# Kernel optimization log

Measured on AMD Instinct MI355X. Metric: run time of the kernel, lower is better.

The kernel has to match this reference:

```python
import jax, jax.numpy as jnp
import numpy as np

L_KERNELS = 15
STRIDE = 1
DIMS = [60, 72, 86, 86, 71, 59]  # indim=4*15, then *1.2,*1.2, mid, /1.2,/1.2 per __init__


def setup_inputs() -> dict:
    key = jax.random.key(0)
    ks = jax.random.split(key, 13)
    B, C, L, K = 16, 4, 1000, 64
    inp = {"x": jax.random.normal(ks[0], (B, C, L), jnp.float32)}
    for i in range(5):
        di, do = DIMS[i], DIMS[i + 1]
        inp[f"w{i}"] = jax.random.normal(ks[1 + 2 * i], (K, di, do), jnp.float32) * (1.0 / np.sqrt(di))
        inp[f"b{i}"] = jax.random.normal(ks[2 + 2 * i], (K, do), jnp.float32) * 0.01
    inp["head_w"] = jax.random.normal(ks[11], (DIMS[5], 1), jnp.float32) * (1.0 / np.sqrt(DIMS[5]))
    inp["head_b"] = jax.random.normal(ks[12], (1,), jnp.float32) * 0.01
    return inp


def reference(x, w0, b0, w1, b1, w2, b2, w3, b3, w4, b4, head_w, head_b):
    B, C, L = x.shape
    l, s = L_KERNELS, STRIDE
    n_out = (L - l) // s + 1
    # unfold: (B, C, n_out, l) via gather of sliding windows
    idx = jnp.arange(n_out)[:, None] * s + jnp.arange(l)[None, :]
    xw = x[:, :, idx]
    # transpose(-2,-3) then flatten(start_dim=3): (B, n_out, C*l)
    xw = jnp.transpose(xw, (0, 2, 1, 3)).reshape(B, n_out, C * l)
    # per-kernel FC stack: broadcast-mul+sum in torch == grouped matmul here
    h = jax.nn.gelu(jnp.einsum('bld,kde->bkle', xw, w0) + b0[None, :, None, :], approximate=False)
    for w, b in ((w1, b1), (w2, b2), (w3, b3), (w4, b4)):
        h = jax.nn.gelu(jnp.einsum('bkld,kde->bkle', h, w) + b[None, :, None, :], approximate=False)
    out = (h @ head_w + head_b).squeeze(-1)  # (B, K, n_out)
    return out
```

## Files before the change

### kernel.cpp

```cpp
#include <hip/hip_runtime.h>

typedef _Float16 f16;
typedef __attribute__((ext_vector_type(8))) _Float16 f16x8;
typedef __attribute__((ext_vector_type(2))) __fp16 hf16x2;
typedef __attribute__((ext_vector_type(4))) float f32x4;

constexpr int C_ = 4, L_ = 1000, K_ = 64, NOUT = 986, NPOS = 16 * 986;
constexpr int TPB  = 256;
constexpr int MTB  = 128;
constexpr int NBLK = (NPOS + MTB - 1) / MTB;
constexpr int AST  = 104;
constexpr int ACT_EL  = MTB * AST;
constexpr size_t SMEM_BYTES = (size_t)ACT_EL * 2 + 480 * 4 + 64 * 4;

constexpr size_t WOFF[5]  = {0, 638976, 1277952, 1916928, 2555904};
constexpr int    WROWS[5] = {80, 96, 96, 80, 64};
constexpr int    DIv[5]   = {60, 72, 86, 86, 71};
constexpr int    DOv[5]   = {72, 86, 86, 71, 59};
constexpr size_t WTOT    = WOFF[4] + (size_t)K_ * 96 * AST;
constexpr size_t ACT_WS  = WTOT;
constexpr size_t WS_NEED = (WTOT + (size_t)NBLK * ACT_EL) * 2;

__device__ __forceinline__ float gelu_f(float x) {
    float x2 = x * x;
    float ei = x * __builtin_fmaf(-0.1029433270f, x2, -2.3022082020f);
    float e  = __builtin_amdgcn_exp2f(ei);
    return x * __builtin_amdgcn_rcpf(e + 1.0f);
}

template<int MT>
__device__ __forceinline__ void pre_a(const f16* __restrict__ wsrc, f16x8 (&ap)[6],
                                      int li, int q) {
#pragma unroll
    for (int mt = 0; mt < MT; mt++)
        ap[mt] = *(const f16x8*)(wsrc + (mt * 16 + li) * AST + q * 8);
}

template<int KSTEPS, int MT>
__device__ __forceinline__ void layer_mm_p(const f16* __restrict__ actw,
                                           const f16* __restrict__ wsrc,
                                           const f16x8 (&ap)[6],
                                           f32x4 (&acc)[MT][2],
                                           const float* __restrict__ bl, int li, int q) {
#pragma unroll
    for (int mt = 0; mt < MT; mt++) {
        f32x4 bb = *(const f32x4*)(bl + mt * 16 + q * 4);
#pragma unroll
        for (int nt = 0; nt < 2; nt++) acc[mt][nt] = bb;
    }
#pragma unroll
    for (int ks = 0; ks < KSTEPS; ks++) {
        const int koff = ks * 32 + q * 8;
        f16x8 a[MT], b[2];
#pragma unroll
        for (int mt = 0; mt < MT; mt++)
            a[mt] = (ks == 0) ? ap[mt]
                              : *(const f16x8*)(wsrc + (mt * 16 + li) * AST + koff);
#pragma unroll
        for (int nt = 0; nt < 2; nt++)
            b[nt] = *(const f16x8*)(actw + (nt * 16 + li) * AST + koff);
#pragma unroll
        for (int mt = 0; mt < MT; mt++)
#pragma unroll
            for (int nt = 0; nt < 2; nt++)
                acc[mt][nt] = __builtin_amdgcn_mfma_f32_16x16x32_f16(a[mt], b[nt], acc[mt][nt], 0, 0, 0);
    }
}

template<int MT>
__device__ __forceinline__ void epilogue(f32x4 (&acc)[MT][2], f16* __restrict__ actw,
                                         int li, int q) {
#pragma unroll
    for (int mt = 0; mt < MT; mt++) {
        const int eb = mt * 16 + q * 4;
#pragma unroll
        for (int nt = 0; nt < 2; nt++) {
            union { hf16x2 h[2]; unsigned long long u; } pk;
            pk.h[0] = __builtin_amdgcn_cvt_pkrtz(gelu_f(acc[mt][nt][0]),
                                                 gelu_f(acc[mt][nt][1]));
            pk.h[1] = __builtin_amdgcn_cvt_pkrtz(gelu_f(acc[mt][nt][2]),
                                                 gelu_f(acc[mt][nt][3]));
            f16* dst = actw + (nt * 16 + li) * AST + eb;
            *(unsigned long long*)dst = pk.u;
        }
    }
}

template<int L>
__device__ __forceinline__ void prep_one(const float* __restrict__ wsrc0, f16* __restrict__ ws,
                                         f16* __restrict__ wl, int k, int tid) {
    constexpr int DI = DIv[L], DO = DOv[L], RW = WROWS[L];
    const float* wsrc = wsrc0 + (size_t)k * DI * DO;
    constexpr int TOT = DI * DO;
    constexpr int NIT = (TOT + 255) / 256;
    float v[NIT];
#pragma unroll
    for (int it = 0; it < NIT; it++) {
        int i = tid + it * 256;
        v[it] = (i < TOT) ? wsrc[i] : 0.f;
    }
#pragma unroll
    for (int it = 0; it < NIT; it++) {
        int i = tid + it * 256;
        if (i < TOT) {
            int d = i / DO, e = i - d * DO;
            wl[d * 87 + e] = (f16)v[it];
        }
    }
    __syncthreads();
    f16* dst = ws + WOFF[L] + (size_t)k * 96 * AST;
    constexpr int CH = RW * 13;
    constexpr int NIT2 = (CH + 255) / 256;
#pragma unroll
    for (int it = 0; it < NIT2; it++) {
        int c = tid + it * 256;
        if (c < CH) {
            int e = c / 13, db = (c - e * 13) * 8;
            f16x8 vv;
#pragma unroll
            for (int j = 0; j < 8; j++) {
                int d = db + j;
                vv[j] = (e < DO && d < DI) ? wl[d * 87 + e] : (f16)0.f;
            }
            *(f16x8*)(dst + (size_t)c * 8) = vv;
        }
    }
}

__device__ __forceinline__ void prep_act(const float* __restrict__ x, f16* __restrict__ dst0,
                                         int m, int tid) {
    f16* dst = dst0 + (size_t)m * ACT_EL;
    const int base = m * MTB;
    for (int i = tid; i < ACT_EL; i += 256) {
        int r = i / AST, c = i - r * AST;
        int p = base + r; if (p > NPOS - 1) p = NPOS - 1;
        int b = p / NOUT, pos = p - b * NOUT;
        float v = 0.f;
        if (c < 60) { int ch = c / 15, j = c - ch * 15; v = x[(size_t)(b * C_ + ch) * L_ + pos + j]; }
        dst[i] = (f16)v;
    }
}

__global__ __launch_bounds__(256) void prep_weights(
    const float* __restrict__ w0, const float* __restrict__ w1, const float* __restrict__ w2,
    const float* __restrict__ w3, const float* __restrict__ w4,
    const float* __restrict__ x, f16* __restrict__ ws) {
    __shared__ f16 wl[86 * 87];
    const int tid = threadIdx.x;
    if (blockIdx.y == 5) { prep_act(x, ws + ACT_WS, blockIdx.x, tid); return; }
    const int k = blockIdx.x;
    if (k >= K_) return;
    switch (blockIdx.y) {
        case 0: prep_one<0>(w0, ws, wl, k, tid); break;
        case 1: prep_one<1>(w1, ws, wl, k, tid); break;
        case 2: prep_one<2>(w2, ws, wl, k, tid); break;
        case 3: prep_one<3>(w3, ws, wl, k, tid); break;
        default: prep_one<4>(w4, ws, wl, k, tid); break;
    }
}

template<bool PRE>
__global__ __launch_bounds__(TPB, 4) void mlp_main(
    const float* __restrict__ x,
    const float* __restrict__ b0, const float* __restrict__ b1, const float* __restrict__ b2,
    const float* __restrict__ b3, const float* __restrict__ b4,
    const float* __restrict__ hw, const float* __restrict__ hb,
    const f16* __restrict__ ws, float* __restrict__ out) {
    extern __shared__ char smemraw[];
    f16*   act   = (f16*)smemraw;
    float* biasl = (float*)(act + ACT_EL);
    float* headl = biasl + 480;

    const int tid = threadIdx.x, k = blockIdx.x, mblk = blockIdx.y;
    const int wv = tid >> 6, lane = tid & 63, li = lane & 15, q = lane >> 4;
    const int base = mblk * MTB;
    f16* actw = act + (wv * 32) * AST;
    const f16* wk = ws + (size_t)k * 96 * AST;

    f16x8 ap[6];
    pre_a<5>(wk + WOFF[0], ap, li, q);

    for (int i = tid; i < 480; i += TPB) {
        int l = i / 96, e = i - l * 96;
        const float* bg = (l == 0) ? b0 : (l == 1) ? b1 : (l == 2) ? b2 : (l == 3) ? b3 : b4;
        int DO = (l == 0) ? 72 : (l == 1) ? 86 : (l == 2) ? 86 : (l == 3) ? 71 : 59;
        biasl[i] = (e < DO) ? bg[k * DO + e] : 0.f;
    }
    if (tid < 64) headl[tid] = (tid < 59) ? hw[tid] : 0.f;

    if constexpr (PRE) {
        const f16* src = ws + ACT_WS + (size_t)mblk * ACT_EL;
        for (int c = wv; c < 26; c += 4) {
            __builtin_amdgcn_global_load_lds(
                (const __attribute__((address_space(1))) void*)(src + c * 512 + lane * 8),
                (__attribute__((address_space(3))) void*)(act + c * 512), 16, 0, 0);
        }
    } else {
        const int b0i = base / NOUT;
        const int thr = (b0i + 1) * NOUT;
        for (int i = tid; i < 64 * MTB; i += TPB) {
            int d = i >> 7, r = i & (MTB - 1);
            int p = base + r; if (p > NPOS - 1) p = NPOS - 1;
            int b = (p >= thr) ? b0i + 1 : b0i;
            int pos = p - b * NOUT;
            float v = 0.f;
            if (d < 60) { int c = d / 15, j = d - c * 15; v = x[(size_t)(b * C_ + c) * L_ + pos + j]; }
            act[r * AST + d] = (f16)v;
        }
        for (int i = tid; i < MTB * 2; i += TPB) {
            int r = i >> 1, cc = (i & 1) << 3;
            *(f16x8*)(act + r * AST + 80 + cc) = f16x8{0,0,0,0,0,0,0,0};
        }
    }
    const float hb0 = hb[0];
    __syncthreads();

    f32x4 acc[6][2];
    f32x4 (&acc5)[5][2] = reinterpret_cast<f32x4 (&)[5][2]>(acc);

    layer_mm_p<2, 5>(actw, wk + WOFF[0], ap, acc5, biasl + 0 * 96, li, q);
    pre_a<6>(wk + WOFF[1], ap, li, q);
    epilogue<5>(acc5, actw, li, q);
    layer_mm_p<3, 6>(actw, wk + WOFF[1], ap, acc, biasl + 1 * 96, li, q);
    pre_a<6>(wk + WOFF[2], ap, li, q);
    epilogue<6>(acc, actw, li, q);
    layer_mm_p<3, 6>(actw, wk + WOFF[2], ap, acc, biasl + 2 * 96, li, q);
    pre_a<5>(wk + WOFF[3], ap, li, q);
    epilogue<6>(acc, actw, li, q);
    layer_mm_p<3, 5>(actw, wk + WOFF[3], ap, acc5, biasl + 3 * 96, li, q);
    pre_a<4>(wk + WOFF[4], ap, li, q);
    epilogue<5>(acc5, actw, li, q);

    f32x4 acc4[4][2];
    layer_mm_p<3, 4>(actw, wk + WOFF[4], ap, acc4, biasl + 4 * 96, li, q);
    float sum[2] = {0.f, 0.f};
#pragma unroll
    for (int mt = 0; mt < 4; mt++) {
        const int eb = mt * 16 + q * 4;
        f32x4 hh = *(const f32x4*)(headl + eb);
#pragma unroll
        for (int nt = 0; nt < 2; nt++) {
#pragma unroll
            for (int r = 0; r < 4; r++)
                sum[nt] += gelu_f(acc4[mt][nt][r]) * hh[r];
        }
    }
#pragma unroll
    for (int nt = 0; nt < 2; nt++) {
        float s = sum[nt];
        s += __shfl_xor(s, 16);
        s += __shfl_xor(s, 32);
        s += hb0;
        if (lane < 16) {
            int p = base + wv * 32 + nt * 16 + lane;
            if (p < NPOS) {
                int b = p / NOUT, pos = p - b * NOUT;
                out[((size_t)(b * K_ + k)) * NOUT + pos] = s;
            }
        }
    }
}

extern "C" void kernel_launch(void* const* d_in, const int* in_sizes, int n_in,
                              void* d_out, int out_size, void* d_ws, size_t ws_size,
                              hipStream_t stream) {
    const float* x  = (const float*)d_in[0];
    const float* w0 = (const float*)d_in[1];  const float* b0 = (const float*)d_in[2];
    const float* w1 = (const float*)d_in[3];  const float* b1 = (const float*)d_in[4];
    const float* w2 = (const float*)d_in[5];  const float* b2 = (const float*)d_in[6];
    const float* w3 = (const float*)d_in[7];  const float* b3 = (const float*)d_in[8];
    const float* w4 = (const float*)d_in[9];  const float* b4 = (const float*)d_in[10];
    const float* hw = (const float*)d_in[11]; const float* hb = (const float*)d_in[12];
    float* out = (float*)d_out;
    f16* ws = (f16*)d_ws;

    const bool pre = (ws_size >= WS_NEED);

    if (pre) {
        (void)hipFuncSetAttribute((const void*)mlp_main<true>,
                                  hipFuncAttributeMaxDynamicSharedMemorySize, (int)SMEM_BYTES);
        prep_weights<<<dim3(NBLK, 6), 256, 0, stream>>>(w0, w1, w2, w3, w4, x, ws);
        mlp_main<true><<<dim3(K_, NBLK), TPB, SMEM_BYTES, stream>>>(
            x, b0, b1, b2, b3, b4, hw, hb, ws, out);
    } else {
        (void)hipFuncSetAttribute((const void*)mlp_main<false>,
                                  hipFuncAttributeMaxDynamicSharedMemorySize, (int)SMEM_BYTES);
        prep_weights<<<dim3(K_, 5), 256, 0, stream>>>(w0, w1, w2, w3, w4, x, ws);
        mlp_main<false><<<dim3(K_, NBLK), TPB, SMEM_BYTES, stream>>>(
            x, b0, b1, b2, b3, b4, hw, hb, ws, out);
    }
}
```

Before: 253.7 us.

## Fuse weight/activation prep and MLP into one persistent cooperative kernel

Replaces the two-launch sequence (prep kernel then main MLP kernel) with a single cooperative persistent kernel. Its blocks first convert weights and activations into the workspace, then do a grid-wide sync, then loop over row tiles with a fixed output channel k per block. The idea is to save a kernel launch and let each block keep its first-layer weight fragments in registers across tiles. It also vectorises activation prep into 8-wide f16 stores. The risks are the cost of the grid sync, less parallelism from the persistent grid being capped at 4 blocks per CU, and a possible occupancy-query failure at launch.

```diff
diff --git a/kernel.cpp b/kernel.cpp
--- a/kernel.cpp
+++ b/kernel.cpp
@@ -1,4 +1,7 @@
 #include <hip/hip_runtime.h>
+#include <hip/hip_cooperative_groups.h>
+
+namespace cg = cooperative_groups;
 
 typedef _Float16 f16;
 typedef __attribute__((ext_vector_type(8))) _Float16 f16x8;
@@ -20,6 +23,9 @@
 constexpr size_t WTOT    = WOFF[4] + (size_t)K_ * 96 * AST;
 constexpr size_t ACT_WS  = WTOT;
 constexpr size_t WS_NEED = (WTOT + (size_t)NBLK * ACT_EL) * 2;
+
+constexpr int NWUNIT = 5 * K_;
+constexpr int NPUNIT = NWUNIT + NBLK;
 
 __device__ __forceinline__ float gelu_f(float x) {
     float x2 = x * x;
@@ -129,15 +135,23 @@
 
 __device__ __forceinline__ void prep_act(const float* __restrict__ x, f16* __restrict__ dst0,
                                          int m, int tid) {
+    if (m >= NBLK) return;
     f16* dst = dst0 + (size_t)m * ACT_EL;
     const int base = m * MTB;
-    for (int i = tid; i < ACT_EL; i += 256) {
-        int r = i / AST, c = i - r * AST;
+    constexpr int CHK = MTB * 13;
+    for (int i = tid; i < CHK; i += 256) {
+        int r = i / 13, cc = (i - r * 13) * 8;
         int p = base + r; if (p > NPOS - 1) p = NPOS - 1;
         int b = p / NOUT, pos = p - b * NOUT;
-        float v = 0.f;
-        if (c < 60) { int ch = c / 15, j = c - ch * 15; v = x[(size_t)(b * C_ + ch) * L_ + pos + j]; }
-        dst[i] = (f16)v;
+        f16x8 vv;
+#pragma unroll
+        for (int j = 0; j < 8; j++) {
+            int c = cc + j;
+            float v = 0.f;
+            if (c < 60) { int ch = c / 15, jj = c - ch * 15; v = x[(size_t)(b * C_ + ch) * L_ + pos + jj]; }
+            vv[j] = (f16)v;
+        }
+        *(f16x8*)(dst + (size_t)r * AST + cc) = vv;
     }
 }
 
@@ -261,6 +275,118 @@
     }
 }
 
+__global__ __launch_bounds__(TPB, 4) void mlp_coop(
+    const float* __restrict__ x,
+    const float* __restrict__ w0, const float* __restrict__ w1, const float* __restrict__ w2,
+    const float* __restrict__ w3, const float* __restrict__ w4,
+    const float* __restrict__ b0, const float* __restrict__ b1, const float* __restrict__ b2,
+    const float* __restrict__ b3, const float* __restrict__ b4,
+    const float* __restrict__ hw, const float* __restrict__ hb,
+    f16* __restrict__ ws, float* __restrict__ out) {
+    extern __shared__ char smemraw[];
+    f16*   act   = (f16*)smemraw;
+    float* biasl = (float*)(act + ACT_EL);
+    float* headl = biasl + 480;
+
+    const int tid = threadIdx.x, bid = blockIdx.x, gsz = gridDim.x;
+
+    for (int u = bid; u < NPUNIT; u += gsz) {
+        if (u < NWUNIT) {
+            const int L = u >> 6, k2 = u & 63;
+            f16* wl = act;
+            switch (L) {
+                case 0: prep_one<0>(w0, ws, wl, k2, tid); break;
+                case 1: prep_one<1>(w1, ws, wl, k2, tid); break;
+                case 2: prep_one<2>(w2, ws, wl, k2, tid); break;
+                case 3: prep_one<3>(w3, ws, wl, k2, tid); break;
+                default: prep_one<4>(w4, ws, wl, k2, tid); break;
+            }
+        } else {
+            prep_act(x, ws + ACT_WS, u - NWUNIT, tid);
+        }
+        __syncthreads();
+    }
+
+    const int k = bid & 63;
+    for (int i = tid; i < 480; i += TPB) {
+        int l = i / 96, e = i - l * 96;
+        const float* bg = (l == 0) ? b0 : (l == 1) ? b1 : (l == 2) ? b2 : (l == 3) ? b3 : b4;
+        int DO = (l == 0) ? 72 : (l == 1) ? 86 : (l == 2) ? 86 : (l == 3) ? 71 : 59;
+        biasl[i] = (e < DO) ? bg[k * DO + e] : 0.f;
+    }
+    if (tid < 64) headl[tid] = (tid < 59) ? hw[tid] : 0.f;
+    const float hb0 = hb[0];
+
+    cg::this_grid().sync();
+
+    const int m0 = bid >> 6, mstep = gsz >> 6;
+    const int wv = tid >> 6, lane = tid & 63, li = lane & 15, q = lane >> 4;
+    f16* actw = act + (wv * 32) * AST;
+    const f16* wk = ws + (size_t)k * 96 * AST;
+
+    f16x8 ap[6];
+    pre_a<5>(wk + WOFF[0], ap, li, q);
+
+    for (int m = m0; m < NBLK; m += mstep) {
+        __syncthreads();
+        const f16* src = ws + ACT_WS + (size_t)m * ACT_EL;
+        for (int c = wv; c < 26; c += 4) {
+            __builtin_amdgcn_global_load_lds(
+                (const __attribute__((address_space(1))) void*)(src + c * 512 + lane * 8),
+                (__attribute__((address_space(3))) void*)(act + c * 512), 16, 0, 0);
+        }
+        __syncthreads();
+
+        f32x4 acc[6][2];
+        f32x4 (&acc5)[5][2] = reinterpret_cast<f32x4 (&)[5][2]>(acc);
+
+        layer_mm_p<2, 5>(actw, wk + WOFF[0], ap, acc5, biasl + 0 * 96, li, q);
+        pre_a<6>(wk + WOFF[1], ap, li, q);
+        epilogue<5>(acc5, actw, li, q);
+        layer_mm_p<3, 6>(actw, wk + WOFF[1], ap, acc, biasl + 1 * 96, li, q);
+        pre_a<6>(wk + WOFF[2], ap, li, q);
+        epilogue<6>(acc, actw, li, q);
+        layer_mm_p<3, 6>(actw, wk + WOFF[2], ap, acc, biasl + 2 * 96, li, q);
+        pre_a<5>(wk + WOFF[3], ap, li, q);
+        epilogue<6>(acc, actw, li, q);
+        layer_mm_p<3, 5>(actw, wk + WOFF[3], ap, acc5, biasl + 3 * 96, li, q);
+        pre_a<4>(wk + WOFF[4], ap, li, q);
+        epilogue<5>(acc5, actw, li, q);
+
+        f32x4 acc4[4][2];
+        layer_mm_p<3, 4>(actw, wk + WOFF[4], ap, acc4, biasl + 4 * 96, li, q);
+        pre_a<5>(wk + WOFF[0], ap, li, q);
+
+        const int base = m * MTB;
+        float sum[2] = {0.f, 0.f};
+#pragma unroll
+        for (int mt = 0; mt < 4; mt++) {
+            const int eb = mt * 16 + q * 4;
+            f32x4 hh = *(const f32x4*)(headl + eb);
+#pragma unroll
+            for (int nt = 0; nt < 2; nt++) {
+#pragma unroll
+                for (int r = 0; r < 4; r++)
+                    sum[nt] += gelu_f(acc4[mt][nt][r]) * hh[r];
+            }
+        }
+#pragma unroll
+        for (int nt = 0; nt < 2; nt++) {
+            float s = sum[nt];
+            s += __shfl_xor(s, 16);
+            s += __shfl_xor(s, 32);
+            s += hb0;
+            if (lane < 16) {
+                int p = base + wv * 32 + nt * 16 + lane;
+                if (p < NPOS) {
+                    int b = p / NOUT, pos = p - b * NOUT;
+                    out[((size_t)(b * K_ + k)) * NOUT + pos] = s;
+                }
+            }
+        }
+    }
+}
+
 extern "C" void kernel_launch(void* const* d_in, const int* in_sizes, int n_in,
                               void* d_out, int out_size, void* d_ws, size_t ws_size,
                               hipStream_t stream) {
@@ -274,9 +400,28 @@
     float* out = (float*)d_out;
     f16* ws = (f16*)d_ws;
 
-    const bool pre = (ws_size >= WS_NEED);
-
-    if (pre) {
+    int dev = 0; (void)hipGetDevice(&dev);
+    int ncu = 0;
+    hipError_t ea = hipDeviceGetAttribute(&ncu, hipDeviceAttributeMultiprocessorCount, dev);
+    int nb = 0;
+    hipError_t eb = hipOccupancyMaxActiveBlocksPerMultiprocessor(
+        &nb, (const void*)mlp_coop, TPB, SMEM_BYTES);
+
+    bool coop = (ea == hipSuccess) && (eb == hipSuccess) &&
+                (ws_size >= WS_NEED) && (ncu > 0) && (nb > 0) && ((size_t)nb * ncu >= 64);
+
+    if (coop) {
+        if (nb > 4) nb = 4;
+        int grid = (nb * ncu / 64) * 64;
+        (void)hipFuncSetAttribute((const void*)mlp_coop,
+                                  hipFuncAttributeMaxDynamicSharedMemorySize, (int)SMEM_BYTES);
+        void* args[] = {(void*)&x,
+                        (void*)&w0, (void*)&w1, (void*)&w2, (void*)&w3, (void*)&w4,
+                        (void*)&b0, (void*)&b1, (void*)&b2, (void*)&b3, (void*)&b4,
+                        (void*)&hw, (void*)&hb, (void*)&ws, (void*)&out};
+        (void)hipLaunchCooperativeKernel((const void*)mlp_coop, dim3(grid), dim3(TPB),
+                                         args, (unsigned)SMEM_BYTES, stream);
+    } else if (ws_size >= WS_NEED) {
         (void)hipFuncSetAttribute((const void*)mlp_main<true>,
                                   hipFuncAttributeMaxDynamicSharedMemorySize, (int)SMEM_BYTES);
         prep_weights<<<dim3(NBLK, 6), 256, 0, stream>>>(w0, w1, w2, w3, w4, x, ws);
```

Measured after the change: 694.3 us. 2.74x slower.

## Split prep work into half-units, vectorize activation prep, raise main kernel occupancy

Applied to the files above, without the earlier changes.

The prep kernel becomes a flat 1-D grid in which each weight layer and activation tile is split into two half-units. This doubles the block count, removes the idle blocks of the old 2-D grid, and spreads the transpose work more evenly. Activation prep now writes 8-wide f16 vectors per thread instead of scalar stores. Separately, the main kernel's launch bounds are raised from 4 to 5 blocks per CU to push occupancy, which risks register spills or a tighter register budget. Each weight half-unit still loads and transposes the full weight matrix through shared memory, so that work is done twice.

```diff
diff --git a/kernel.cpp b/kernel.cpp
--- a/kernel.cpp
+++ b/kernel.cpp
@@ -20,6 +20,9 @@
 constexpr size_t WTOT    = WOFF[4] + (size_t)K_ * 96 * AST;
 constexpr size_t ACT_WS  = WTOT;
 constexpr size_t WS_NEED = (WTOT + (size_t)NBLK * ACT_EL) * 2;
+
+constexpr int WUNITS = 5 * K_ * 2;
+constexpr int AUNITS = NBLK * 2;
 
 __device__ __forceinline__ float gelu_f(float x) {
     float x2 = x * x;
@@ -87,8 +90,9 @@
 }
 
 template<int L>
-__device__ __forceinline__ void prep_one(const float* __restrict__ wsrc0, f16* __restrict__ ws,
-                                         f16* __restrict__ wl, int k, int tid) {
+__device__ __forceinline__ void prep_one_half(const float* __restrict__ wsrc0,
+                                              f16* __restrict__ ws, f16* __restrict__ wl,
+                                              int k, int h, int tid) {
     constexpr int DI = DIv[L], DO = DOv[L], RW = WROWS[L];
     const float* wsrc = wsrc0 + (size_t)k * DI * DO;
     constexpr int TOT = DI * DO;
@@ -109,12 +113,13 @@
     }
     __syncthreads();
     f16* dst = ws + WOFF[L] + (size_t)k * 96 * AST;
-    constexpr int CH = RW * 13;
-    constexpr int NIT2 = (CH + 255) / 256;
+    constexpr int HCH = (RW / 2) * 13;
+    constexpr int NIT2 = (HCH + 255) / 256;
 #pragma unroll
     for (int it = 0; it < NIT2; it++) {
-        int c = tid + it * 256;
-        if (c < CH) {
+        int c0 = tid + it * 256;
+        if (c0 < HCH) {
+            int c = h * HCH + c0;
             int e = c / 13, db = (c - e * 13) * 8;
             f16x8 vv;
 #pragma unroll
@@ -127,40 +132,52 @@
     }
 }
 
-__device__ __forceinline__ void prep_act(const float* __restrict__ x, f16* __restrict__ dst0,
-                                         int m, int tid) {
+__device__ __forceinline__ void prep_act_half(const float* __restrict__ x,
+                                              f16* __restrict__ dst0, int m, int h, int tid) {
+    if (m >= NBLK) return;
     f16* dst = dst0 + (size_t)m * ACT_EL;
     const int base = m * MTB;
-    for (int i = tid; i < ACT_EL; i += 256) {
-        int r = i / AST, c = i - r * AST;
+    constexpr int HCHK = MTB * 13 / 2;
+    for (int i0 = tid; i0 < HCHK; i0 += 256) {
+        int i = h * HCHK + i0;
+        int r = i / 13, cc = (i - r * 13) * 8;
         int p = base + r; if (p > NPOS - 1) p = NPOS - 1;
         int b = p / NOUT, pos = p - b * NOUT;
-        float v = 0.f;
-        if (c < 60) { int ch = c / 15, j = c - ch * 15; v = x[(size_t)(b * C_ + ch) * L_ + pos + j]; }
-        dst[i] = (f16)v;
-    }
-}
-
-__global__ __launch_bounds__(256) void prep_weights(
+        f16x8 vv;
+#pragma unroll
+        for (int j = 0; j < 8; j++) {
+            int c = cc + j;
+            float v = 0.f;
+            if (c < 60) { int ch = c / 15, jj = c - ch * 15; v = x[(size_t)(b * C_ + ch) * L_ + pos + jj]; }
+            vv[j] = (f16)v;
+        }
+        *(f16x8*)(dst + (size_t)r * AST + cc) = vv;
+    }
+}
+
+__global__ __launch_bounds__(256) void prep_all(
     const float* __restrict__ w0, const float* __restrict__ w1, const float* __restrict__ w2,
     const float* __restrict__ w3, const float* __restrict__ w4,
     const float* __restrict__ x, f16* __restrict__ ws) {
     __shared__ f16 wl[86 * 87];
-    const int tid = threadIdx.x;
-    if (blockIdx.y == 5) { prep_act(x, ws + ACT_WS, blockIdx.x, tid); return; }
-    const int k = blockIdx.x;
-    if (k >= K_) return;
-    switch (blockIdx.y) {
-        case 0: prep_one<0>(w0, ws, wl, k, tid); break;
-        case 1: prep_one<1>(w1, ws, wl, k, tid); break;
-        case 2: prep_one<2>(w2, ws, wl, k, tid); break;
-        case 3: prep_one<3>(w3, ws, wl, k, tid); break;
-        default: prep_one<4>(w4, ws, wl, k, tid); break;
+    const int tid = threadIdx.x, u = blockIdx.x;
+    if (u < WUNITS) {
+        const int k = (u >> 1) & 63, h = u & 1;
+        switch (u >> 7) {
+            case 0: prep_one_half<0>(w0, ws, wl, k, h, tid); break;
+            case 1: prep_one_half<1>(w1, ws, wl, k, h, tid); break;
+            case 2: prep_one_half<2>(w2, ws, wl, k, h, tid); break;
+            case 3: prep_one_half<3>(w3, ws, wl, k, h, tid); break;
+            default: prep_one_half<4>(w4, ws, wl, k, h, tid); break;
+        }
+    } else {
+        const int v = u - WUNITS;
+        prep_act_half(x, ws + ACT_WS, v >> 1, v & 1, tid);
     }
 }
 
 template<bool PRE>
-__global__ __launch_bounds__(TPB, 4) void mlp_main(
+__global__ __launch_bounds__(TPB, 5) void mlp_main(
     const float* __restrict__ x,
     const float* __restrict__ b0, const float* __restrict__ b1, const float* __restrict__ b2,
     const float* __restrict__ b3, const float* __restrict__ b4,
@@ -279,13 +296,13 @@
     if (pre) {
         (void)hipFuncSetAttribute((const void*)mlp_main<true>,
                                   hipFuncAttributeMaxDynamicSharedMemorySize, (int)SMEM_BYTES);
-        prep_weights<<<dim3(NBLK, 6), 256, 0, stream>>>(w0, w1, w2, w3, w4, x, ws);
+        prep_all<<<dim3(WUNITS + AUNITS), 256, 0, stream>>>(w0, w1, w2, w3, w4, x, ws);
         mlp_main<true><<<dim3(K_, NBLK), TPB, SMEM_BYTES, stream>>>(
             x, b0, b1, b2, b3, b4, hw, hb, ws, out);
     } else {
         (void)hipFuncSetAttribute((const void*)mlp_main<false>,
                                   hipFuncAttributeMaxDynamicSharedMemorySize, (int)SMEM_BYTES);
-        prep_weights<<<dim3(K_, 5), 256, 0, stream>>>(w0, w1, w2, w3, w4, x, ws);
+        prep_all<<<dim3(WUNITS), 256, 0, stream>>>(w0, w1, w2, w3, w4, x, ws);
         mlp_main<false><<<dim3(K_, NBLK), TPB, SMEM_BYTES, stream>>>(
             x, b0, b1, b2, b3, b4, hw, hb, ws, out);
     }
```

After: 253.6 us. No clear change (-0.0%).
